# Kernel optimization log

Measured on AMD Instinct MI355X. Metric: run time of the kernel, lower is better.

The kernel has to match this reference:

```python
import jax, jax.numpy as jnp
import numpy as np

D_MODEL = 1024
H = 16
D_K = D_MODEL // H


def setup_inputs() -> dict:
    key = jax.random.key(0)
    ks = jax.random.split(key, 12)
    B, S = 2, 2048
    inp = {
        "q": jax.random.normal(ks[0], (B, S, D_MODEL), jnp.float32),
        "k": jax.random.normal(ks[1], (B, S, D_MODEL), jnp.float32),
        "v": jax.random.normal(ks[2], (B, S, D_MODEL), jnp.float32),
        "mask": jax.random.randint(ks[3], (1, 1, S, S), 0, 2, jnp.int32),
    }
    s = 1.0 / np.sqrt(D_MODEL)
    inp["wq_w"] = jax.random.normal(ks[4], (D_MODEL, D_MODEL), jnp.float32) * s
    inp["wq_b"] = jnp.zeros((D_MODEL,), jnp.float32)
    inp["wk_w"] = jax.random.normal(ks[5], (D_MODEL, D_MODEL), jnp.float32) * s
    inp["wk_b"] = jnp.zeros((D_MODEL,), jnp.float32)
    inp["wv_w"] = jax.random.normal(ks[6], (D_MODEL, D_MODEL), jnp.float32) * s
    inp["wv_b"] = jnp.zeros((D_MODEL,), jnp.float32)
    inp["wo_w"] = jax.random.normal(ks[7], (D_MODEL, D_MODEL), jnp.float32) * s
    inp["wo_b"] = jnp.zeros((D_MODEL,), jnp.float32)
    return inp


def reference(q, k, v, mask, wq_w, wq_b, wk_w, wk_b, wv_w, wv_b, wo_w, wo_b):
    B, S, _ = q.shape
    # projections (torch Linear: x @ W^T + b)
    def proj(x, w, b):
        y = x @ w.T + b
        return y.reshape(B, S, H, D_K).transpose(0, 2, 1, 3)  # [B,H,S,Dk]

    Q = proj(q, wq_w, wq_b)
    K = proj(k, wk_w, wk_b)
    V = proj(v, wv_w, wv_b)

    scores = jnp.einsum("bhqd,bhkd->bhqk", Q, K) / jnp.sqrt(jnp.float32(D_K))
    # source quirk: masked positions set to 1e-9 (NOT -inf) before softmax
    scores = jnp.where(mask == 0, jnp.float32(1e-9), scores)
    attn = jax.nn.softmax(scores, axis=-1)
    out = jnp.einsum("bhqk,bhkd->bhqd", attn, V)
    out = out.transpose(0, 2, 1, 3).reshape(B, S, H * D_K)
    return out @ wo_w.T + wo_b
```

## Files before the change

### kernel.cpp

```cpp
#include <hip/hip_runtime.h>

typedef _Float16 half_t;
typedef _Float16 h8 __attribute__((ext_vector_type(8)));
typedef _Float16 h4 __attribute__((ext_vector_type(4)));
typedef _Float16 h2 __attribute__((ext_vector_type(2)));
typedef float f32x4 __attribute__((ext_vector_type(4)));
typedef float f32x16 __attribute__((ext_vector_type(16)));

#define S_LEN 2048
#define DMODEL 1024
#define NHEAD 16
#define HDK 64
#define NB 2
#define MROWS (NB * S_LEN)
#define LOG2E 1.44269504089f

__device__ __forceinline__ void gload_lds16(const void* g, void* l) {
  __builtin_amdgcn_global_load_lds(
      (const __attribute__((address_space(1))) unsigned int*)g,
      (__attribute__((address_space(3))) unsigned int*)l, 16, 0, 0);
}

__device__ __forceinline__ float fast_exp2(float x) {
  float r;
  asm("v_exp_f32 %0, %1" : "=v"(r) : "v"(x));
  return r;
}

__device__ __forceinline__ int swz(int row, int colByte) {
  return row * 128 + (colByte ^ ((row & 7) << 4));
}

__global__ __launch_bounds__(256) void pre_kernel(
    const float* __restrict__ q, const float* __restrict__ k, const float* __restrict__ v,
    const float* __restrict__ wq, const float* __restrict__ wk,
    const float* __restrict__ wv, const float* __restrict__ wo,
    const int* __restrict__ mask,
    half_t* Xq, half_t* Xk, half_t* Xv,
    half_t* Wq, half_t* Wk, half_t* Wv, half_t* Wo,
    unsigned int* mbits) {
  const int gid = blockIdx.x, tid = threadIdx.x;
  if (gid < 16384) {
    int i = gid * 256 + tid;
    const float* src; half_t* dst; int off;
    if (i < 3145728) {
      int rgn = i >> 20; off = i & 1048575;
      src = rgn == 0 ? q : rgn == 1 ? k : v;
      dst = rgn == 0 ? Xq : rgn == 1 ? Xk : Xv;
    } else {
      int j = i - 3145728;
      int rgn = j >> 18; off = j & 262143;
      src = rgn == 0 ? wq : rgn == 1 ? wk : rgn == 2 ? wv : wo;
      dst = rgn == 0 ? Wq : rgn == 1 ? Wk : rgn == 2 ? Wv : Wo;
    }
    float4 vv = ((const float4*)src)[off];
    h4 o;
    o[0] = (half_t)vv.x; o[1] = (half_t)vv.y; o[2] = (half_t)vv.z; o[3] = (half_t)vv.w;
    ((h4*)dst)[off] = o;
  } else {
    int i = (gid - 16384) * 256 + tid;
    int mv = mask[i];
    unsigned long long bm = __ballot(mv != 0);
    int lane = tid & 63;
    if (lane == 0)       mbits[i >> 5] = (unsigned int)bm;
    else if (lane == 32) mbits[i >> 5] = (unsigned int)(bm >> 32);
  }
}

template <int EPI>
__global__ __launch_bounds__(256) void gemm_kernel(
    const half_t* __restrict__ A0, const half_t* __restrict__ A1, const half_t* __restrict__ A2,
    const half_t* __restrict__ W0, const half_t* __restrict__ W1, const half_t* __restrict__ W2,
    const float* __restrict__ b0, const float* __restrict__ b1, const float* __restrict__ b2,
    void* o0, void* o1, void* o2) {
  const half_t* A; const half_t* W; const float* bias; void* out; float scale;
  if (blockIdx.z == 0)      { A = A0; W = W0; bias = b0; out = o0; scale = (EPI == 0) ? 0.125f * LOG2E : 1.0f; }
  else if (blockIdx.z == 1) { A = A1; W = W1; bias = b1; out = o1; scale = 1.0f; }
  else                      { A = A2; W = W2; bias = b2; out = o2; scale = 1.0f; }

  __shared__ half_t As[128 * 64];
  __shared__ half_t Bs[128 * 64];
  const int tid = threadIdx.x;
  const int w = tid >> 6, lane = tid & 63;
  const int wm = w >> 1, wn = w & 1;
  const int bm = blockIdx.x, bn = blockIdx.y;

  f32x4 acc[4][4] = {};

  const int r8 = lane >> 3;
  const int scb2 = ((lane & 7) * 16) ^ (r8 << 4);
  const char* Ab = (const char*)A + (size_t)(bm * 128) * 2048;
  const char* Wb = (const char*)W + (size_t)(bn * 128) * 2048;
  char* AsB = (char*)As;
  char* BsB = (char*)Bs;

  const int rr = lane & 15;
  const int kgB = (lane >> 4) * 16;
  const int swzr = (rr & 7) << 4;

  for (int kb0 = 0; kb0 < 2048; kb0 += 128) {
    __syncthreads();
#pragma unroll
    for (int p = 0; p < 4; ++p) {
      const int row = p * 32 + w * 8 + r8;
      const size_t srow = (size_t)row * 2048 + kb0 + scb2;
      gload_lds16(Ab + srow, AsB + (p * 32 + w * 8) * 128);
      gload_lds16(Wb + srow, BsB + (p * 32 + w * 8) * 128);
    }
    __syncthreads();

#pragma unroll
    for (int h = 0; h < 2; ++h) {
      const int kcb = (kgB + h * 64) ^ swzr;
      h8 af[4], bf[4];
#pragma unroll
      for (int i = 0; i < 4; ++i) {
        af[i] = *(const h8*)(AsB + (wm * 64 + i * 16 + rr) * 128 + kcb);
        bf[i] = *(const h8*)(BsB + (wn * 64 + i * 16 + rr) * 128 + kcb);
      }
#pragma unroll
      for (int i = 0; i < 4; ++i)
#pragma unroll
        for (int j = 0; j < 4; ++j)
          acc[i][j] = __builtin_amdgcn_mfma_f32_16x16x32_f16(af[i], bf[j], acc[i][j], 0, 0, 0);
    }
  }

  const int r0 = bm * 128 + wm * 64;
  const int c0 = bn * 128 + wn * 64;
#pragma unroll
  for (int j = 0; j < 4; ++j) {
    int col = c0 + j * 16 + (lane & 15);
    float bc = bias[col];
#pragma unroll
    for (int i = 0; i < 4; ++i) {
#pragma unroll
      for (int jj = 0; jj < 4; ++jj) {
        int row = r0 + i * 16 + (lane >> 4) * 4 + jj;
        float val = acc[i][j][jj] + bc;
        if (EPI == 0) {
          int bb = row >> 11, s = row & (S_LEN - 1);
          int hh = col >> 6, dk = col & 63;
          if (blockIdx.z == 2) {
            ((half_t*)out)[((size_t)((bb * NHEAD + hh) * HDK + dk)) * S_LEN + s] = (half_t)val;
          } else {
            ((half_t*)out)[(((size_t)(bb * NHEAD + hh)) * S_LEN + s) * HDK + dk] =
                (half_t)(val * scale);
          }
        } else {
          ((float*)out)[(size_t)row * DMODEL + col] = val;
        }
      }
    }
  }
}

__global__ __launch_bounds__(256, 4) void attn_kernel(
    const half_t* __restrict__ Qp, const half_t* __restrict__ Kp,
    const half_t* __restrict__ VTp, const unsigned int* __restrict__ mbits,
    half_t* __restrict__ AO) {
  __shared__ char smem[32768];

  const int tid = threadIdx.x, w = tid >> 6, lane = tid & 63;
  const int qg = w >> 1, kh = w & 1;
  const int id = blockIdx.x;
  const int xcd = id & 7, rest = id >> 3;
  const int bh = (xcd << 2) | (rest >> 5);
  const int qt = rest & 31;
  const int b = bh >> 4, h = bh & 15;
  const int q32 = lane & 31, hi = lane >> 5;
  const int qbase = qt * 64 + qg * 32;
  const half_t* Qb = Qp + (size_t)bh * (S_LEN * HDK);
  const char* Kb = (const char*)(Kp + (size_t)bh * (S_LEN * HDK));
  const char* VTb = (const char*)(VTp + (size_t)bh * (S_LEN * HDK));
  const unsigned int* mrow = mbits + (size_t)(qbase + q32) * (S_LEN / 32);

  char* Ks = smem;
  char* Vs = smem + 16384;
  const int srow = w * 16 + (lane >> 3);
  const int scb = (lane & 7) * 16;

  h8 qf[4];
#pragma unroll
  for (int s = 0; s < 4; ++s)
    qf[s] = *(const h8*)(Qb + (size_t)(qbase + q32) * HDK + s * 16 + hi * 8);

  f32x16 acc0 = {}, acc1 = {};
  float l_run = 0.f;

  unsigned int mw = mrow[kh];
#pragma unroll
  for (int p = 0; p < 2; ++p) {
    int r = srow + p * 8;
    gload_lds16(Kb + (size_t)r * 128 + (scb ^ ((r & 7) << 4)),
                Ks + (w * 16 + p * 8) * 128);
    gload_lds16(VTb + (size_t)r * (S_LEN * 2) + (scb ^ ((r & 7) << 4)),
                Vs + (w * 16 + p * 8) * 128);
  }
  __syncthreads();

  int cur = 0;
  for (int t = 0; t < 32; ++t) {
    const unsigned int mwc = mw >> (hi * 4);

    if (t < 31) {
      const int kvn = t + 1;
#pragma unroll
      for (int p = 0; p < 2; ++p) {
        int r = srow + p * 8;
        gload_lds16(Kb + (size_t)(kvn * 64 + r) * 128 + (scb ^ ((r & 7) << 4)),
                    Ks + (cur ^ 1) * 8192 + (w * 16 + p * 8) * 128);
        gload_lds16(VTb + (size_t)r * (S_LEN * 2) + kvn * 128 + (scb ^ ((r & 7) << 4)),
                    Vs + (cur ^ 1) * 8192 + (w * 16 + p * 8) * 128);
      }
      mw = mrow[kvn * 2 + kh];
    }

    const char* kb = Ks + cur * 8192;
    const char* vb = Vs + cur * 8192;
    f32x16 sc = {};
    __builtin_amdgcn_s_setprio(1);
#pragma unroll
    for (int s = 0; s < 4; ++s) {
      h8 kf = *(const h8*)(kb + swz(kh * 32 + q32, s * 32 + hi * 16));
      sc = __builtin_amdgcn_mfma_f32_32x32x16_f16(kf, qf[s], sc, 0, 0, 0);
    }
    __builtin_amdgcn_s_setprio(0);

    h8 vf00 = *(const h8*)(vb + swz(q32, kh * 64 + hi * 16));
    h8 vf01 = *(const h8*)(vb + swz(q32, kh * 64 + 32 + hi * 16));
    h8 vf10 = *(const h8*)(vb + swz(32 + q32, kh * 64 + hi * 16));
    h8 vf11 = *(const h8*)(vb + swz(32 + q32, kh * 64 + 32 + hi * 16));

#pragma unroll
    for (int rg = 0; rg < 16; ++rg) {
      const int bit = (rg & 3) + 8 * (rg >> 2);
      float p = fast_exp2(((mwc >> bit) & 1u) ? sc[rg] : 0.0f);
      sc[rg] = p;
      l_run += p;
    }

    h8 pb[2];
#pragma unroll
    for (int s = 0; s < 2; ++s) {
      const int rb = s * 8;
      union { h2 h; unsigned int u; } c01, c23, c45, c67;
      c01.h[0] = (half_t)sc[rb + 0]; c01.h[1] = (half_t)sc[rb + 1];
      c23.h[0] = (half_t)sc[rb + 2]; c23.h[1] = (half_t)sc[rb + 3];
      c45.h[0] = (half_t)sc[rb + 4]; c45.h[1] = (half_t)sc[rb + 5];
      c67.h[0] = (half_t)sc[rb + 6]; c67.h[1] = (half_t)sc[rb + 7];
      auto rA = __builtin_amdgcn_permlane32_swap(c01.u, c45.u, false, false);
      auto rB = __builtin_amdgcn_permlane32_swap(c23.u, c67.u, false, false);
      union { unsigned int u[4]; h8 v; } bw;
      bw.u[0] = rA[0]; bw.u[1] = rB[0]; bw.u[2] = rA[1]; bw.u[3] = rB[1];
      pb[s] = bw.v;
    }

    __builtin_amdgcn_s_setprio(1);
    acc0 = __builtin_amdgcn_mfma_f32_32x32x16_f16(vf00, pb[0], acc0, 0, 0, 0);
    acc1 = __builtin_amdgcn_mfma_f32_32x32x16_f16(vf10, pb[0], acc1, 0, 0, 0);
    acc0 = __builtin_amdgcn_mfma_f32_32x32x16_f16(vf01, pb[1], acc0, 0, 0, 0);
    acc1 = __builtin_amdgcn_mfma_f32_32x32x16_f16(vf11, pb[1], acc1, 0, 0, 0);
    __builtin_amdgcn_s_setprio(0);

    __syncthreads();
    cur ^= 1;
  }

  float* my = (float*)smem + (qg * 64 + lane) * 33;
  if (kh) {
#pragma unroll
    for (int rg = 0; rg < 16; ++rg) { my[rg] = acc0[rg]; my[16 + rg] = acc1[rg]; }
    my[32] = l_run;
  }
  __syncthreads();
  if (!kh) {
#pragma unroll
    for (int rg = 0; rg < 16; ++rg) { acc0[rg] += my[rg]; acc1[rg] += my[16 + rg]; }
    l_run += my[32];
    l_run += __shfl_xor(l_run, 32);

    const float inv = 1.0f / l_run;
    const int qrow = qbase + q32;
    half_t* aob = AO + (size_t)(b * S_LEN + qrow) * DMODEL + h * HDK;
#pragma unroll
    for (int rq = 0; rq < 4; ++rq) {
      h4 s0, s1;
#pragma unroll
      for (int j = 0; j < 4; ++j) {
        s0[j] = (half_t)(acc0[rq * 4 + j] * inv);
        s1[j] = (half_t)(acc1[rq * 4 + j] * inv);
      }
      const int d0 = 8 * rq + 4 * hi;
      *(h4*)(aob + d0) = s0;
      *(h4*)(aob + 32 + d0) = s1;
    }
  }
}

extern "C" void kernel_launch(void* const* d_in, const int* in_sizes, int n_in,
                              void* d_out, int out_size, void* d_ws, size_t ws_size,
                              hipStream_t stream) {
  const float* q    = (const float*)d_in[0];
  const float* k    = (const float*)d_in[1];
  const float* v    = (const float*)d_in[2];
  const int*   mask = (const int*)d_in[3];
  const float* wq_w = (const float*)d_in[4];
  const float* wq_b = (const float*)d_in[5];
  const float* wk_w = (const float*)d_in[6];
  const float* wk_b = (const float*)d_in[7];
  const float* wv_w = (const float*)d_in[8];
  const float* wv_b = (const float*)d_in[9];
  const float* wo_w = (const float*)d_in[10];
  const float* wo_b = (const float*)d_in[11];
  float* out = (float*)d_out;

  char* ws = (char*)d_ws;
  const size_t MB = (size_t)1 << 20;
  half_t* Xq = (half_t*)(ws + 0 * MB);
  half_t* Xk = (half_t*)(ws + 8 * MB);
  half_t* Xv = (half_t*)(ws + 16 * MB);
  half_t* Wq = (half_t*)(ws + 24 * MB);
  half_t* Wk = (half_t*)(ws + 26 * MB);
  half_t* Wv = (half_t*)(ws + 28 * MB);
  half_t* Wo = (half_t*)(ws + 30 * MB);
  half_t* Qp = (half_t*)(ws + 32 * MB);
  half_t* Kp = (half_t*)(ws + 40 * MB);
  half_t* VT = (half_t*)(ws + 48 * MB);
  unsigned int* mbits = (unsigned int*)(ws + 56 * MB);
  half_t* AO = Xq;

  pre_kernel<<<32768, 256, 0, stream>>>(q, k, v, wq_w, wk_w, wv_w, wo_w, mask,
                                        Xq, Xk, Xv, Wq, Wk, Wv, Wo, mbits);
  gemm_kernel<0><<<dim3(32, 8, 3), 256, 0, stream>>>(
      Xq, Xk, Xv, Wq, Wk, Wv, wq_b, wk_b, wv_b, (void*)Qp, (void*)Kp, (void*)VT);
  attn_kernel<<<1024, 256, 0, stream>>>(Qp, Kp, VT, mbits, AO);
  gemm_kernel<1><<<dim3(32, 8, 1), 256, 0, stream>>>(
      AO, AO, AO, Wo, Wo, Wo, wo_b, wo_b, wo_b, (void*)out, (void*)out, (void*)out);

  (void)in_sizes; (void)n_in; (void)out_size; (void)ws_size;
}
```

Before: 156.7 us.

## Double-buffer GEMM LDS tiles and remap blocks across XCDs

The projection GEMM now uses two LDS buffers of K=32 tiles and issues the global-to-LDS load for the next tile before computing on the current one, so each step needs one barrier instead of two and memory latency can overlap MFMA work. The grid becomes 1D, with block IDs remapped so consecutive tiles land on the same XCD, which should improve L2 reuse of the A and W rows. In exchange each LDS stage is smaller, so there are more loop iterations and barriers, and the swizzle has to match the new 64-byte row pitch.

```diff
diff --git a/kernel.cpp b/kernel.cpp
--- a/kernel.cpp
+++ b/kernel.cpp
@@ -73,58 +73,71 @@
     const half_t* __restrict__ W0, const half_t* __restrict__ W1, const half_t* __restrict__ W2,
     const float* __restrict__ b0, const float* __restrict__ b1, const float* __restrict__ b2,
     void* o0, void* o1, void* o2) {
+  const int nwg = gridDim.x;
+  const int cpx = nwg >> 3;
+  const int id = blockIdx.x;
+  const int nid = (id & 7) * cpx + (id >> 3);
+  const int z = nid >> 8;
+  const int rmn = nid & 255;
+  const int bm = rmn >> 3, bn = rmn & 7;
+
   const half_t* A; const half_t* W; const float* bias; void* out; float scale;
-  if (blockIdx.z == 0)      { A = A0; W = W0; bias = b0; out = o0; scale = (EPI == 0) ? 0.125f * LOG2E : 1.0f; }
-  else if (blockIdx.z == 1) { A = A1; W = W1; bias = b1; out = o1; scale = 1.0f; }
-  else                      { A = A2; W = W2; bias = b2; out = o2; scale = 1.0f; }
-
-  __shared__ half_t As[128 * 64];
-  __shared__ half_t Bs[128 * 64];
+  if (z == 0)      { A = A0; W = W0; bias = b0; out = o0; scale = (EPI == 0) ? 0.125f * LOG2E : 1.0f; }
+  else if (z == 1) { A = A1; W = W1; bias = b1; out = o1; scale = 1.0f; }
+  else             { A = A2; W = W2; bias = b2; out = o2; scale = 1.0f; }
+
+  __shared__ half_t As[2][128 * 32];
+  __shared__ half_t Bs[2][128 * 32];
   const int tid = threadIdx.x;
   const int w = tid >> 6, lane = tid & 63;
   const int wm = w >> 1, wn = w & 1;
-  const int bm = blockIdx.x, bn = blockIdx.y;
+  const int crow = lane >> 2;
+  const int ckb = ((lane & 3) * 16) ^ ((crow & 3) << 4);
 
   f32x4 acc[4][4] = {};
 
-  const int r8 = lane >> 3;
-  const int scb2 = ((lane & 7) * 16) ^ (r8 << 4);
-  const char* Ab = (const char*)A + (size_t)(bm * 128) * 2048;
-  const char* Wb = (const char*)W + (size_t)(bn * 128) * 2048;
-  char* AsB = (char*)As;
-  char* BsB = (char*)Bs;
+  const char* Ar0 = (const char*)A + (size_t)(bm * 128 + w * 16 + crow) * 2048 + ckb;
+  const char* Ar1 = Ar0 + 64 * 2048;
+  const char* Wr0 = (const char*)W + (size_t)(bn * 128 + w * 16 + crow) * 2048 + ckb;
+  const char* Wr1 = Wr0 + 64 * 2048;
 
   const int rr = lane & 15;
-  const int kgB = (lane >> 4) * 16;
-  const int swzr = (rr & 7) << 4;
-
-  for (int kb0 = 0; kb0 < 2048; kb0 += 128) {
+  const int kkB = (lane >> 4) * 16;
+  const int kswz = (rr & 3) << 4;
+
+#define GSTAGE(buf, ktB)                                     \
+  do {                                                       \
+    gload_lds16(Ar0 + (ktB), As[buf] + w * 512);             \
+    gload_lds16(Ar1 + (ktB), As[buf] + (w + 4) * 512);       \
+    gload_lds16(Wr0 + (ktB), Bs[buf] + w * 512);             \
+    gload_lds16(Wr1 + (ktB), Bs[buf] + (w + 4) * 512);       \
+  } while (0)
+
+  GSTAGE(0, 0);
+  __syncthreads();
+
+  int cur = 0;
+  for (int ktB = 0; ktB < 2048; ktB += 64) {
+    if (ktB + 64 < 2048) GSTAGE(cur ^ 1, ktB + 64);
+
+    const char* AsB = (const char*)As[cur];
+    const char* BsB = (const char*)Bs[cur];
+    h8 af[4], bf[4];
+#pragma unroll
+    for (int i = 0; i < 4; ++i) {
+      af[i] = *(const h8*)(AsB + (wm * 64 + i * 16 + rr) * 64 + (kkB ^ kswz));
+      bf[i] = *(const h8*)(BsB + (wn * 64 + i * 16 + rr) * 64 + (kkB ^ kswz));
+    }
+#pragma unroll
+    for (int i = 0; i < 4; ++i)
+#pragma unroll
+      for (int j = 0; j < 4; ++j)
+        acc[i][j] = __builtin_amdgcn_mfma_f32_16x16x32_f16(af[i], bf[j], acc[i][j], 0, 0, 0);
+
     __syncthreads();
-#pragma unroll
-    for (int p = 0; p < 4; ++p) {
-      const int row = p * 32 + w * 8 + r8;
-      const size_t srow = (size_t)row * 2048 + kb0 + scb2;
-      gload_lds16(Ab + srow, AsB + (p * 32 + w * 8) * 128);
-      gload_lds16(Wb + srow, BsB + (p * 32 + w * 8) * 128);
-    }
-    __syncthreads();
-
-#pragma unroll
-    for (int h = 0; h < 2; ++h) {
-      const int kcb = (kgB + h * 64) ^ swzr;
-      h8 af[4], bf[4];
-#pragma unroll
-      for (int i = 0; i < 4; ++i) {
-        af[i] = *(const h8*)(AsB + (wm * 64 + i * 16 + rr) * 128 + kcb);
-        bf[i] = *(const h8*)(BsB + (wn * 64 + i * 16 + rr) * 128 + kcb);
-      }
-#pragma unroll
-      for (int i = 0; i < 4; ++i)
-#pragma unroll
-        for (int j = 0; j < 4; ++j)
-          acc[i][j] = __builtin_amdgcn_mfma_f32_16x16x32_f16(af[i], bf[j], acc[i][j], 0, 0, 0);
-    }
-  }
+    cur ^= 1;
+  }
+#undef GSTAGE
 
   const int r0 = bm * 128 + wm * 64;
   const int c0 = bn * 128 + wn * 64;
@@ -141,7 +154,7 @@
         if (EPI == 0) {
           int bb = row >> 11, s = row & (S_LEN - 1);
           int hh = col >> 6, dk = col & 63;
-          if (blockIdx.z == 2) {
+          if (z == 2) {
             ((half_t*)out)[((size_t)((bb * NHEAD + hh) * HDK + dk)) * S_LEN + s] = (half_t)val;
           } else {
             ((half_t*)out)[(((size_t)(bb * NHEAD + hh)) * S_LEN + s) * HDK + dk] =
@@ -332,10 +345,10 @@
 
   pre_kernel<<<32768, 256, 0, stream>>>(q, k, v, wq_w, wk_w, wv_w, wo_w, mask,
                                         Xq, Xk, Xv, Wq, Wk, Wv, Wo, mbits);
-  gemm_kernel<0><<<dim3(32, 8, 3), 256, 0, stream>>>(
+  gemm_kernel<0><<<768, 256, 0, stream>>>(
       Xq, Xk, Xv, Wq, Wk, Wv, wq_b, wk_b, wv_b, (void*)Qp, (void*)Kp, (void*)VT);
   attn_kernel<<<1024, 256, 0, stream>>>(Qp, Kp, VT, mbits, AO);
-  gemm_kernel<1><<<dim3(32, 8, 1), 256, 0, stream>>>(
+  gemm_kernel<1><<<256, 256, 0, stream>>>(
       AO, AO, AO, Wo, Wo, Wo, wo_b, wo_b, wo_b, (void*)out, (void*)out, (void*)out);
 
   (void)in_sizes; (void)n_in; (void)out_size; (void)ws_size;
```

Result: faster. 152.2 us (-2.9%).
